# Kernel tuning notes

Hardware: AMD Instinct MI355X
Metric: run time of the kernel (lower is better)

Reference implementation:

```python
import jax, jax.numpy as jnp
import numpy as np

N_NODES = 100000
N_EDGES = 20000
NNZ = 800000
D_IN = 256
D_OUT = 256


def _segment_mean(feats, seg_ids, num_segments):
    # feats: [nnz, d] gathered features; seg_ids: [nnz] target segment per entry
    s = jax.ops.segment_sum(feats, seg_ids, num_segments=num_segments)
    cnt = jax.ops.segment_sum(jnp.ones((seg_ids.shape[0],), feats.dtype), seg_ids,
                              num_segments=num_segments)
    return s / jnp.maximum(cnt, 1.0)[:, None]


def setup_inputs() -> dict:
    key = jax.random.key(0)
    k1, k2, k3, k4, k5 = jax.random.split(key, 5)
    X = jax.random.normal(k1, (N_NODES, D_IN), dtype=jnp.float32)
    W = jax.random.normal(k2, (D_IN, D_OUT), dtype=jnp.float32) * (1.0 / np.sqrt(D_IN))
    b = jax.random.normal(k3, (D_OUT,), dtype=jnp.float32) * 0.01
    vertex_idx = jax.random.randint(k4, (NNZ,), 0, N_NODES, dtype=jnp.int32)
    edge_idx = jax.random.randint(k5, (NNZ,), 0, N_EDGES, dtype=jnp.int32)
    return {"X": X, "W": W, "b": b, "vertex_idx": vertex_idx, "edge_idx": edge_idx}


def reference(X, W, b, vertex_idx, edge_idx):
    # theta: linear projection
    H = X @ W + b                                   # [N_NODES, D_OUT]
    # v2e mean: hyperedge feature = mean of incident vertex features
    Y = _segment_mean(H[vertex_idx], edge_idx, N_EDGES)   # [N_EDGES, D_OUT]
    # e2v mean: vertex feature = mean of incident hyperedge features
    X_ = _segment_mean(Y[edge_idx], vertex_idx, N_NODES)  # [N_NODES, D_OUT]
    # ReLU; dropout is identity in eval mode
    return jax.nn.relu(X_)
```

## Files before the change

### kernel.cpp

```cpp
#include <hip/hip_runtime.h>
#include <hip/hip_bf16.h>

constexpr int N_NODES = 100000;
constexpr int N_EDGES = 20000;
constexpr int NNZ     = 800000;
constexpr int D       = 256;

typedef unsigned short ushort_t;
typedef unsigned short ushort4v __attribute__((ext_vector_type(4)));
typedef unsigned short ushort8v __attribute__((ext_vector_type(8)));
typedef __bf16         bf16x8   __attribute__((ext_vector_type(8)));
typedef float          f32x4    __attribute__((ext_vector_type(4)));
typedef float          f32x8    __attribute__((ext_vector_type(8)));
typedef unsigned long long u64;
typedef unsigned long long u64x2 __attribute__((ext_vector_type(2)));

static __device__ inline ushort_t f2bf(float f) {
  unsigned u = __builtin_bit_cast(unsigned, f);
  return (ushort_t)((u + 0x7FFFu + ((u >> 16) & 1u)) >> 16);
}

static __device__ inline f32x8 row_f32(const ushort_t* p) {
  bf16x8 b = __builtin_bit_cast(bf16x8, *(const ushort8v*)p);
  return __builtin_convertvector(b, f32x8);
}

static __device__ inline int bsum(u64 x) {
  return (int)((x * 0x0101010101010101ULL) >> 56);
}

constexpr int HCHUNKS   = 32;
constexpr int CHUNK4    = NNZ / 4 / HCHUNKS;
constexpr int PWORDS    = HCHUNKS / 8;
constexpr int NH_RANGES = 5;
constexpr int NH_BINS   = N_NODES / NH_RANGES;
constexpr int NH_BLOCKS = NH_RANGES * HCHUNKS;
constexpr int EH_BLOCKS = HCHUNKS;
constexpr int HIST_BLOCKS  = NH_BLOCKS + EH_BLOCKS;
constexpr int TRANS_BLOCKS = 64;
constexpr int PREP_BLOCKS  = HIST_BLOCKS + TRANS_BLOCKS;
constexpr int HWORDS = 5000;

__global__ __launch_bounds__(256) void prep_kernel(
    const float* __restrict__ W,
    const int* __restrict__ vidx, const int* __restrict__ eidx,
    ushort_t* __restrict__ Wt,
    unsigned char* __restrict__ pe, unsigned char* __restrict__ pn,
    unsigned char* __restrict__ lre, unsigned char* __restrict__ lrn) {
  __shared__ unsigned int hist[HWORDS];
  const int blk = blockIdx.x, tid = threadIdx.x;
  if (blk < HIST_BLOCKS) {
    const bool is_n = blk < NH_BLOCKS;
    const int c  = is_n ? (blk & (HCHUNKS - 1)) : (blk - NH_BLOCKS);
    const int lo = is_n ? (blk >> 5) * NH_BINS : 0;
    const int* __restrict__ idx = is_n ? vidx : eidx;
    unsigned char* __restrict__ lr = is_n ? lrn : lre;
    for (int t = tid; t < HWORDS; t += 256) hist[t] = 0;
    __syncthreads();
    const int base4 = c * CHUNK4;
    for (int k = tid; k < CHUNK4; k += 256) {
      int i4 = base4 + k;
      int4 q = ((const int4*)idx)[i4];
      int vv[4] = {q.x, q.y, q.z, q.w};
#pragma unroll
      for (int j = 0; j < 4; ++j) {
        unsigned rel = (unsigned)(vv[j] - lo);
        if (rel < (unsigned)NH_BINS) {
          unsigned sh = 8u * (rel & 3u);
          unsigned old = atomicAdd(&hist[rel >> 2], 1u << sh);
          lr[(size_t)i4 * 4 + j] = (unsigned char)((old >> sh) & 0xFFu);
        }
      }
    }
    __syncthreads();
    unsigned char* __restrict__ pb = is_n ? pn : pe;
    for (int t = tid; t < NH_BINS; t += 256) {
      unsigned byte = (hist[t >> 2] >> (8u * (t & 3u))) & 0xFFu;
      pb[(size_t)(lo + t) * HCHUNKS + c] = (unsigned char)byte;
    }
  } else {
    int wb = blk - HIST_BLOCKS;
#pragma unroll
    for (int i = 0; i < 4; ++i) {
      int k = wb * 4 + i;
      Wt[(size_t)tid * 256 + k] = f2bf(W[(size_t)k * 256 + tid]);
    }
  }
}

constexpr int SCAN_L    = N_EDGES + N_NODES;
constexpr int SCAN_TPB  = 1024;
constexpr int SCAN_EPT  = 4;
constexpr int SCAN_TILE = SCAN_TPB * SCAN_EPT;
constexpr int SCAN_NB   = (SCAN_L + SCAN_TILE - 1) / SCAN_TILE;

static __device__ inline int bsum32(const u64* P) {
  u64x2 a = *(const u64x2*)P;
  u64x2 b = *(const u64x2*)(P + 2);
  return bsum(a[0]) + bsum(a[1]) + bsum(b[0]) + bsum(b[1]);
}

__global__ __launch_bounds__(1024) void scan_phaseA(
    const u64* __restrict__ pe, const u64* __restrict__ pn,
    int* __restrict__ comb, int* __restrict__ btot) {
  __shared__ int wsum[16];
  const int tid = threadIdx.x, lane = tid & 63, wid = tid >> 6;
  const int base = blockIdx.x * SCAN_TILE + tid * SCAN_EPT;
  int v[SCAN_EPT];
#pragma unroll
  for (int i = 0; i < SCAN_EPT; ++i) {
    int j = base + i;
    int x = 0;
    if (j < SCAN_L)
      x = bsum32(j < N_EDGES ? pe + (size_t)j * PWORDS
                             : pn + (size_t)(j - N_EDGES) * PWORDS);
    v[i] = x;
  }
  int tsum = v[0] + v[1] + v[2] + v[3];
  int x = tsum;
#pragma unroll
  for (int d = 1; d < 64; d <<= 1) {
    int y = __shfl_up(x, (unsigned)d, 64);
    if (lane >= d) x += y;
  }
  if (lane == 63) wsum[wid] = x;
  __syncthreads();
  if (wid == 0) {
    int s = (lane < 16) ? wsum[lane] : 0;
#pragma unroll
    for (int d = 1; d < 16; d <<= 1) {
      int y = __shfl_up(s, (unsigned)d, 64);
      if (lane >= d) s += y;
    }
    if (lane < 16) wsum[lane] = s;
  }
  __syncthreads();
  int texcl = ((wid == 0) ? 0 : wsum[wid - 1]) + (x - tsum);
  int run = texcl;
#pragma unroll
  for (int i = 0; i < SCAN_EPT; ++i) {
    int j = base + i;
    if (j < SCAN_L) comb[j] = run;
    run += v[i];
  }
  if (tid == 0) btot[blockIdx.x] = wsum[15];
}

__global__ __launch_bounds__(1024) void scan_phaseC(
    const int* __restrict__ comb, const int* __restrict__ btot,
    int* __restrict__ eoff, int* __restrict__ noff) {
  int add = 0;
  for (int bdx = 0; bdx < blockIdx.x; ++bdx) add += btot[bdx];
  const int base = blockIdx.x * SCAN_TILE + threadIdx.x * SCAN_EPT;
#pragma unroll
  for (int i = 0; i < SCAN_EPT; ++i) {
    int j = base + i;
    if (j < SCAN_L) {
      int val = comb[j] + add;
      if (j < N_EDGES) eoff[j] = val;
      else             noff[j - N_EDGES] = val - NNZ;
    }
  }
  if (blockIdx.x == 0 && threadIdx.x == 0) {
    eoff[N_EDGES] = NNZ;
    noff[N_NODES] = NNZ;
  }
}

__global__ __launch_bounds__(256) void scatter_calc(
    const int* __restrict__ vidx, const int* __restrict__ eidx,
    const int* __restrict__ eoff, const int* __restrict__ noff,
    const u64* __restrict__ pe, const u64* __restrict__ pn,
    const unsigned char* __restrict__ lre, const unsigned char* __restrict__ lrn,
    int* __restrict__ evals, int* __restrict__ nvals) {
  int i4 = blockIdx.x * 256 + threadIdx.x;
  if (i4 >= NNZ / 4) return;
  int c = i4 / CHUNK4;
  int w = c >> 3, sub = c & 7;
  u64 mw = (1ULL << (8 * sub)) - 1ULL;
  u64 m0 = (w > 0) ? ~0ULL : mw;
  u64 m1 = (w > 1) ? ~0ULL : ((w == 1) ? mw : 0ULL);
  u64 m2 = (w > 2) ? ~0ULL : ((w == 2) ? mw : 0ULL);
  u64 m3 = (w == 3) ? mw : 0ULL;
  int4 e4 = ((const int4*)eidx)[i4];
  int4 v4 = ((const int4*)vidx)[i4];
  unsigned le = *(const unsigned*)(lre + (size_t)i4 * 4);
  unsigned ln = *(const unsigned*)(lrn + (size_t)i4 * 4);
  int ee[4] = {e4.x, e4.y, e4.z, e4.w};
  int vv[4] = {v4.x, v4.y, v4.z, v4.w};
#pragma unroll
  for (int j = 0; j < 4; ++j) {
    int e = ee[j], v = vv[j];
    u64x2 ea = *(const u64x2*)(pe + (size_t)e * PWORDS);
    u64x2 eb = *(const u64x2*)(pe + (size_t)e * PWORDS + 2);
    u64x2 na = *(const u64x2*)(pn + (size_t)v * PWORDS);
    u64x2 nb = *(const u64x2*)(pn + (size_t)v * PWORDS + 2);
    int pre_e = bsum(ea[0] & m0) + bsum(ea[1] & m1) + bsum(eb[0] & m2) + bsum(eb[1] & m3);
    int pre_n = bsum(na[0] & m0) + bsum(na[1] & m1) + bsum(nb[0] & m2) + bsum(nb[1] & m3);
    int re = (int)((le >> (8 * j)) & 0xFFu);
    int rn = (int)((ln >> (8 * j)) & 0xFFu);
    evals[eoff[e] + pre_e + re] = v;
    nvals[noff[v] + pre_n + rn] = e;
  }
}

__global__ __launch_bounds__(256) void v2e_mean_f32(
    const float* __restrict__ X, const int* __restrict__ eoff,
    const int* __restrict__ evals, ushort_t* __restrict__ Xeb) {
  int wave = threadIdx.x >> 6, lane = threadIdx.x & 63;
  int seg = blockIdx.x * 4 + wave;
  int s = eoff[seg], e = eoff[seg + 1];
  const float* base = X + lane * 4;
  f32x4 a0 = {0, 0, 0, 0}, a1 = a0, a2 = a0, a3 = a0;
  int j = s;
  for (; j + 3 < e; j += 4) {
    int r0 = evals[j], r1 = evals[j + 1], r2 = evals[j + 2], r3 = evals[j + 3];
    a0 += *(const f32x4*)&base[(size_t)r0 * 256];
    a1 += *(const f32x4*)&base[(size_t)r1 * 256];
    a2 += *(const f32x4*)&base[(size_t)r2 * 256];
    a3 += *(const f32x4*)&base[(size_t)r3 * 256];
  }
  for (; j < e; ++j)
    a0 += *(const f32x4*)&base[(size_t)evals[j] * 256];
  a0 = (a0 + a1) + (a2 + a3);
  float inv = 1.0f / (float)max(e - s, 1);
  ushort4v o;
#pragma unroll
  for (int i = 0; i < 4; ++i) o[i] = f2bf(a0[i] * inv);
  *(ushort4v*)&Xeb[(size_t)seg * 256 + lane * 4] = o;
}

__global__ __launch_bounds__(256) void gemm_mfma(
    const ushort_t* __restrict__ A, const ushort_t* __restrict__ Wt,
    const float* __restrict__ bias, ushort_t* __restrict__ Ye) {
  const int w = threadIdx.x >> 6, lane = threadIdx.x & 63;
  const int m15 = lane & 15, q = lane >> 4;
  const int m0 = blockIdx.x * 16;
  const ushort_t* arow = A + (size_t)(m0 + m15) * 256 + q * 8;
  f32x4 acc[4] = { {0,0,0,0}, {0,0,0,0}, {0,0,0,0}, {0,0,0,0} };
  for (int k0 = 0; k0 < 256; k0 += 32) {
    bf16x8 af = __builtin_bit_cast(bf16x8, *(const ushort8v*)(arow + k0));
#pragma unroll
    for (int t = 0; t < 4; ++t) {
      const ushort_t* brow = Wt + (size_t)(w * 64 + t * 16 + m15) * 256 + k0 + q * 8;
      bf16x8 bf = __builtin_bit_cast(bf16x8, *(const ushort8v*)brow);
      acc[t] = __builtin_amdgcn_mfma_f32_16x16x32_bf16(af, bf, acc[t], 0, 0, 0);
    }
  }
#pragma unroll
  for (int t = 0; t < 4; ++t) {
    int col = w * 64 + t * 16 + m15;
    float bv = bias[col];
#pragma unroll
    for (int r = 0; r < 4; ++r) {
      int row = m0 + q * 4 + r;
      Ye[(size_t)row * 256 + col] = f2bf(acc[t][r] + bv);
    }
  }
}

__global__ __launch_bounds__(256) void e2v_mean_relu(
    const ushort_t* __restrict__ Yeb, const int* __restrict__ noff,
    const int* __restrict__ nvals, float* __restrict__ dst) {
  int half = threadIdx.x >> 5, l32 = threadIdx.x & 31;
  int seg = blockIdx.x * 8 + half;
  int s = noff[seg], e = noff[seg + 1];
  const ushort_t* base = Yeb + l32 * 8;
  f32x8 a0 = {0, 0, 0, 0, 0, 0, 0, 0}, a1 = a0;
  int j = s;
  for (; j + 1 < e; j += 2) {
    int r0 = nvals[j], r1 = nvals[j + 1];
    a0 += row_f32(&base[(size_t)r0 * 256]);
    a1 += row_f32(&base[(size_t)r1 * 256]);
  }
  if (j < e) a0 += row_f32(&base[(size_t)nvals[j] * 256]);
  a0 += a1;
  float inv = 1.0f / (float)max(e - s, 1);
  float4 o0, o1;
  o0.x = fmaxf(a0[0] * inv, 0.f); o0.y = fmaxf(a0[1] * inv, 0.f);
  o0.z = fmaxf(a0[2] * inv, 0.f); o0.w = fmaxf(a0[3] * inv, 0.f);
  o1.x = fmaxf(a0[4] * inv, 0.f); o1.y = fmaxf(a0[5] * inv, 0.f);
  o1.z = fmaxf(a0[6] * inv, 0.f); o1.w = fmaxf(a0[7] * inv, 0.f);
  size_t b = (size_t)seg * 256 + l32 * 8;
  *(float4*)&dst[b]     = o0;
  *(float4*)&dst[b + 4] = o1;
}

constexpr size_t OFF_XEB   = 0;
constexpr size_t OFF_YEB   = OFF_XEB + (size_t)N_EDGES * D * 2;
constexpr size_t OFF_WT    = OFF_YEB + (size_t)N_EDGES * D * 2;
constexpr size_t OFF_PE    = OFF_WT  + (size_t)D * D * 2;
constexpr size_t OFF_PN    = OFF_PE  + (size_t)N_EDGES * HCHUNKS;
constexpr size_t OFF_LRE   = OFF_PN  + (size_t)N_NODES * HCHUNKS;
constexpr size_t OFF_LRN   = OFF_LRE + (size_t)NNZ;
constexpr size_t OFF_EOFF  = OFF_LRN + (size_t)NNZ;
constexpr size_t OFF_NOFF  = OFF_EOFF + (size_t)(N_EDGES + 1 + 3) * 4;
constexpr size_t OFF_EVALS = OFF_NOFF + (size_t)(N_NODES + 1 + 3) * 4;
constexpr size_t OFF_NVALS = OFF_EVALS + (size_t)NNZ * 4;
constexpr size_t OFF_COMB  = OFF_NVALS + (size_t)NNZ * 4;
constexpr size_t OFF_BTOT  = OFF_COMB + (size_t)SCAN_L * 4;

extern "C" void kernel_launch(void* const* d_in, const int* in_sizes, int n_in,
                              void* d_out, int out_size, void* d_ws, size_t ws_size,
                              hipStream_t stream) {
  const float* X    = (const float*)d_in[0];
  const float* W    = (const float*)d_in[1];
  const float* b    = (const float*)d_in[2];
  const int*   vidx = (const int*)d_in[3];
  const int*   eidx = (const int*)d_in[4];
  float*       out  = (float*)d_out;

  char* ws = (char*)d_ws;
  ushort_t* Xeb  = (ushort_t*)(ws + OFF_XEB);
  ushort_t* Yeb  = (ushort_t*)(ws + OFF_YEB);
  ushort_t* Wt   = (ushort_t*)(ws + OFF_WT);
  unsigned char* pe_b = (unsigned char*)(ws + OFF_PE);
  unsigned char* pn_b = (unsigned char*)(ws + OFF_PN);
  u64* pe_u = (u64*)(ws + OFF_PE);
  u64* pn_u = (u64*)(ws + OFF_PN);
  unsigned char* lre = (unsigned char*)(ws + OFF_LRE);
  unsigned char* lrn = (unsigned char*)(ws + OFF_LRN);
  int* eoff  = (int*)(ws + OFF_EOFF);
  int* noff  = (int*)(ws + OFF_NOFF);
  int* evals = (int*)(ws + OFF_EVALS);
  int* nvals = (int*)(ws + OFF_NVALS);
  int* comb  = (int*)(ws + OFF_COMB);
  int* btot  = (int*)(ws + OFF_BTOT);


  prep_kernel<<<PREP_BLOCKS, 256, 0, stream>>>(W, vidx, eidx, Wt,
                                               pe_b, pn_b, lre, lrn);

  scan_phaseA<<<SCAN_NB, SCAN_TPB, 0, stream>>>(pe_u, pn_u, comb, btot);
  scan_phaseC<<<SCAN_NB, SCAN_TPB, 0, stream>>>(comb, btot, eoff, noff);

  scatter_calc<<<(NNZ / 4 + 255) / 256, 256, 0, stream>>>(
      vidx, eidx, eoff, noff, pe_u, pn_u, lre, lrn, evals, nvals);

  v2e_mean_f32<<<N_EDGES / 4, 256, 0, stream>>>(X, eoff, evals, Xeb);

  gemm_mfma<<<N_EDGES / 16, 256, 0, stream>>>(Xeb, Wt, b, Yeb);

  e2v_mean_relu<<<N_NODES / 8, 256, 0, stream>>>(Yeb, noff, nvals, out);
}
```

Measured before the change: 421.9 us.

## Project all nodes with GEMM first, then gather bf16 H for v2e mean

Reorders the computation so the linear projection runs on all node features up front, writing a bf16 H, and the v2e segment mean gathers bf16 rows of H instead of fp32 rows of X. This halves the bytes per gathered row in the v2e stage. The cost is a GEMM over all nodes instead of only the edge rows, plus writing and reading a full bf16 H buffer. The e2v loop is also unrolled to four accumulators.

```diff
diff --git a/kernel.cpp b/kernel.cpp
--- a/kernel.cpp
+++ b/kernel.cpp
@@ -204,59 +204,66 @@
   }
 }
 
-__global__ __launch_bounds__(256) void v2e_mean_f32(
-    const float* __restrict__ X, const int* __restrict__ eoff,
-    const int* __restrict__ evals, ushort_t* __restrict__ Xeb) {
-  int wave = threadIdx.x >> 6, lane = threadIdx.x & 63;
-  int seg = blockIdx.x * 4 + wave;
+__global__ __launch_bounds__(256) void gemm_h(
+    const float* __restrict__ X, const ushort_t* __restrict__ Wt,
+    const float* __restrict__ bias, ushort_t* __restrict__ H) {
+  const int w = threadIdx.x >> 6, lane = threadIdx.x & 63;
+  const int m15 = lane & 15, q = lane >> 4;
+  const int m0 = blockIdx.x * 32 + (w >> 1) * 16;
+  const int c0 = (w & 1) * 128;
+  const float* xrow = X + (size_t)(m0 + m15) * 256 + q * 8;
+  f32x4 acc[8] = { {0,0,0,0}, {0,0,0,0}, {0,0,0,0}, {0,0,0,0},
+                   {0,0,0,0}, {0,0,0,0}, {0,0,0,0}, {0,0,0,0} };
+  for (int k0 = 0; k0 < 256; k0 += 32) {
+    f32x4 xa = *(const f32x4*)(xrow + k0);
+    f32x4 xb = *(const f32x4*)(xrow + k0 + 4);
+    ushort8v au;
+    au[0] = f2bf(xa[0]); au[1] = f2bf(xa[1]); au[2] = f2bf(xa[2]); au[3] = f2bf(xa[3]);
+    au[4] = f2bf(xb[0]); au[5] = f2bf(xb[1]); au[6] = f2bf(xb[2]); au[7] = f2bf(xb[3]);
+    bf16x8 af = __builtin_bit_cast(bf16x8, au);
+#pragma unroll
+    for (int t = 0; t < 8; ++t) {
+      const ushort_t* brow = Wt + (size_t)(c0 + t * 16 + m15) * 256 + k0 + q * 8;
+      bf16x8 bf = __builtin_bit_cast(bf16x8, *(const ushort8v*)brow);
+      acc[t] = __builtin_amdgcn_mfma_f32_16x16x32_bf16(af, bf, acc[t], 0, 0, 0);
+    }
+  }
+#pragma unroll
+  for (int t = 0; t < 8; ++t) {
+    int col = c0 + t * 16 + m15;
+    float bv = bias[col];
+#pragma unroll
+    for (int r = 0; r < 4; ++r) {
+      int row = m0 + q * 4 + r;
+      H[(size_t)row * 256 + col] = f2bf(acc[t][r] + bv);
+    }
+  }
+}
+
+__global__ __launch_bounds__(256) void v2e_mean(
+    const ushort_t* __restrict__ H, const int* __restrict__ eoff,
+    const int* __restrict__ evals, ushort_t* __restrict__ Yeb) {
+  int half = threadIdx.x >> 5, l32 = threadIdx.x & 31;
+  int seg = blockIdx.x * 8 + half;
   int s = eoff[seg], e = eoff[seg + 1];
-  const float* base = X + lane * 4;
-  f32x4 a0 = {0, 0, 0, 0}, a1 = a0, a2 = a0, a3 = a0;
+  const ushort_t* base = H + l32 * 8;
+  f32x8 a0 = {0, 0, 0, 0, 0, 0, 0, 0}, a1 = a0, a2 = a0, a3 = a0;
   int j = s;
   for (; j + 3 < e; j += 4) {
     int r0 = evals[j], r1 = evals[j + 1], r2 = evals[j + 2], r3 = evals[j + 3];
-    a0 += *(const f32x4*)&base[(size_t)r0 * 256];
-    a1 += *(const f32x4*)&base[(size_t)r1 * 256];
-    a2 += *(const f32x4*)&base[(size_t)r2 * 256];
-    a3 += *(const f32x4*)&base[(size_t)r3 * 256];
+    a0 += row_f32(&base[(size_t)r0 * 256]);
+    a1 += row_f32(&base[(size_t)r1 * 256]);
+    a2 += row_f32(&base[(size_t)r2 * 256]);
+    a3 += row_f32(&base[(size_t)r3 * 256]);
   }
   for (; j < e; ++j)
-    a0 += *(const f32x4*)&base[(size_t)evals[j] * 256];
+    a0 += row_f32(&base[(size_t)evals[j] * 256]);
   a0 = (a0 + a1) + (a2 + a3);
   float inv = 1.0f / (float)max(e - s, 1);
-  ushort4v o;
-#pragma unroll
-  for (int i = 0; i < 4; ++i) o[i] = f2bf(a0[i] * inv);
-  *(ushort4v*)&Xeb[(size_t)seg * 256 + lane * 4] = o;
-}
-
-__global__ __launch_bounds__(256) void gemm_mfma(
-    const ushort_t* __restrict__ A, const ushort_t* __restrict__ Wt,
-    const float* __restrict__ bias, ushort_t* __restrict__ Ye) {
-  const int w = threadIdx.x >> 6, lane = threadIdx.x & 63;
-  const int m15 = lane & 15, q = lane >> 4;
-  const int m0 = blockIdx.x * 16;
-  const ushort_t* arow = A + (size_t)(m0 + m15) * 256 + q * 8;
-  f32x4 acc[4] = { {0,0,0,0}, {0,0,0,0}, {0,0,0,0}, {0,0,0,0} };
-  for (int k0 = 0; k0 < 256; k0 += 32) {
-    bf16x8 af = __builtin_bit_cast(bf16x8, *(const ushort8v*)(arow + k0));
-#pragma unroll
-    for (int t = 0; t < 4; ++t) {
-      const ushort_t* brow = Wt + (size_t)(w * 64 + t * 16 + m15) * 256 + k0 + q * 8;
-      bf16x8 bf = __builtin_bit_cast(bf16x8, *(const ushort8v*)brow);
-      acc[t] = __builtin_amdgcn_mfma_f32_16x16x32_bf16(af, bf, acc[t], 0, 0, 0);
-    }
-  }
-#pragma unroll
-  for (int t = 0; t < 4; ++t) {
-    int col = w * 64 + t * 16 + m15;
-    float bv = bias[col];
-#pragma unroll
-    for (int r = 0; r < 4; ++r) {
-      int row = m0 + q * 4 + r;
-      Ye[(size_t)row * 256 + col] = f2bf(acc[t][r] + bv);
-    }
-  }
+  ushort8v o;
+#pragma unroll
+  for (int i = 0; i < 8; ++i) o[i] = f2bf(a0[i] * inv);
+  *(ushort8v*)&Yeb[(size_t)seg * 256 + l32 * 8] = o;
 }
 
 __global__ __launch_bounds__(256) void e2v_mean_relu(
@@ -266,15 +273,18 @@
   int seg = blockIdx.x * 8 + half;
   int s = noff[seg], e = noff[seg + 1];
   const ushort_t* base = Yeb + l32 * 8;
-  f32x8 a0 = {0, 0, 0, 0, 0, 0, 0, 0}, a1 = a0;
+  f32x8 a0 = {0, 0, 0, 0, 0, 0, 0, 0}, a1 = a0, a2 = a0, a3 = a0;
   int j = s;
-  for (; j + 1 < e; j += 2) {
-    int r0 = nvals[j], r1 = nvals[j + 1];
+  for (; j + 3 < e; j += 4) {
+    int r0 = nvals[j], r1 = nvals[j + 1], r2 = nvals[j + 2], r3 = nvals[j + 3];
     a0 += row_f32(&base[(size_t)r0 * 256]);
     a1 += row_f32(&base[(size_t)r1 * 256]);
-  }
-  if (j < e) a0 += row_f32(&base[(size_t)nvals[j] * 256]);
-  a0 += a1;
+    a2 += row_f32(&base[(size_t)r2 * 256]);
+    a3 += row_f32(&base[(size_t)r3 * 256]);
+  }
+  for (; j < e; ++j)
+    a0 += row_f32(&base[(size_t)nvals[j] * 256]);
+  a0 = (a0 + a1) + (a2 + a3);
   float inv = 1.0f / (float)max(e - s, 1);
   float4 o0, o1;
   o0.x = fmaxf(a0[0] * inv, 0.f); o0.y = fmaxf(a0[1] * inv, 0.f);
@@ -286,8 +296,8 @@
   *(float4*)&dst[b + 4] = o1;
 }
 
-constexpr size_t OFF_XEB   = 0;
-constexpr size_t OFF_YEB   = OFF_XEB + (size_t)N_EDGES * D * 2;
+constexpr size_t OFF_H     = 0;
+constexpr size_t OFF_YEB   = OFF_H   + (size_t)N_NODES * D * 2;
 constexpr size_t OFF_WT    = OFF_YEB + (size_t)N_EDGES * D * 2;
 constexpr size_t OFF_PE    = OFF_WT  + (size_t)D * D * 2;
 constexpr size_t OFF_PN    = OFF_PE  + (size_t)N_EDGES * HCHUNKS;
@@ -311,7 +321,7 @@
   float*       out  = (float*)d_out;
 
   char* ws = (char*)d_ws;
-  ushort_t* Xeb  = (ushort_t*)(ws + OFF_XEB);
+  ushort_t* H    = (ushort_t*)(ws + OFF_H);
   ushort_t* Yeb  = (ushort_t*)(ws + OFF_YEB);
   ushort_t* Wt   = (ushort_t*)(ws + OFF_WT);
   unsigned char* pe_b = (unsigned char*)(ws + OFF_PE);
@@ -331,15 +341,15 @@
   prep_kernel<<<PREP_BLOCKS, 256, 0, stream>>>(W, vidx, eidx, Wt,
                                                pe_b, pn_b, lre, lrn);
 
+  gemm_h<<<N_NODES / 32, 256, 0, stream>>>(X, Wt, b, H);
+
   scan_phaseA<<<SCAN_NB, SCAN_TPB, 0, stream>>>(pe_u, pn_u, comb, btot);
   scan_phaseC<<<SCAN_NB, SCAN_TPB, 0, stream>>>(comb, btot, eoff, noff);
 
   scatter_calc<<<(NNZ / 4 + 255) / 256, 256, 0, stream>>>(
       vidx, eidx, eoff, noff, pe_u, pn_u, lre, lrn, evals, nvals);
 
-  v2e_mean_f32<<<N_EDGES / 4, 256, 0, stream>>>(X, eoff, evals, Xeb);
-
-  gemm_mfma<<<N_EDGES / 16, 256, 0, stream>>>(Xeb, Wt, b, Yeb);
+  v2e_mean<<<N_EDGES / 8, 256, 0, stream>>>(H, eoff, evals, Yeb);
 
   e2v_mean_relu<<<N_NODES / 8, 256, 0, stream>>>(Yeb, noff, nvals, out);
 }
```

After: 479.9 us. 13.8% more time.
